# Kernel tuning notes

Measured on AMD Instinct MI355X. Metric: run time of the kernel, lower is better.

## Reference

```python
import jax, jax.numpy as jnp
import numpy as np

K = 5
PAD = 2  # same-size output: pad = dilation*(k-1)/2


def _patches(x, k, pad):
    # x: [B, C, H, W] -> [B, C, k, k, H', W'] (matches torch F.unfold + view layout)
    B, C, H, W = x.shape
    p = jax.lax.conv_general_dilated_patches(
        x, (k, k), (1, 1), [(pad, pad), (pad, pad)])
    return p.reshape(B, C, k, k, p.shape[-2], p.shape[-1])


def setup_inputs() -> dict:
    key = jax.random.key(0)
    k1, k2, k3, k4 = jax.random.split(key, 4)
    B, Cin, Cout, Cg, H, W = 4, 32, 32, 8, 128, 128
    x = jax.random.normal(k1, (B, Cin, H, W), jnp.float32)
    guide = jax.random.normal(k2, (B, Cg, H, W), jnp.float32)
    weight = jax.random.normal(k3, (Cout, Cin, K, K), jnp.float32) * 0.05
    bias = jax.random.normal(k4, (Cout,), jnp.float32) * 0.05
    return {"x": x, "guide": guide, "weight": weight, "bias": bias}


def reference(x, guide, weight, bias):
    k = weight.shape[-1]
    # --- packernel2d (gaussian, smooth_kernel_type='none', channel_wise=False) ---
    gp = _patches(guide, k, PAD)                      # [B, Cg, k, k, H, W]
    center = gp[:, :, k // 2, k // 2][:, :, None, None]  # self-tap feature
    d = gp - center
    kernel = jnp.exp(-0.5 * jnp.sum(d * d, axis=1, keepdims=True))  # [B,1,k,k,H,W]
    # --- pacconv2d native path ---
    cols = _patches(x, k, PAD)                        # [B, Cin, k, k, H, W]
    out = jnp.einsum('bjklmn,ojkl->bomn', cols * kernel, weight)
    return out + bias[None, :, None, None]
```

## Files before the change

kernel.cpp:

```cpp
#include <hip/hip_runtime.h>

#define Bn   4
#define CIN  32
#define COUT 32
#define CG   8
#define Hh   128
#define Ww   128
#define KK   5
#define HW   (Hh * Ww)

#define TW   64
#define TH   4
#define PRW  68
#define PRH  8
#define NSLOT (PRW * PRH)

typedef _Float16 h8  __attribute__((ext_vector_type(8)));
typedef _Float16 h2  __attribute__((ext_vector_type(2)));
typedef float    f4  __attribute__((ext_vector_type(4)));

#define XOFF  0
#define XJG   8704
#define WOFF  34816
#define KOFF  60416
#define SMEMB 73216

#define XT_OFF 0
#define WT_OFF 4194304
#define KW_OFF 4245504
#define WS_NEED 7522304

__global__ __launch_bounds__(512) void prep(
    const float* __restrict__ x, const float* __restrict__ guide,
    const float* __restrict__ w,
    _Float16* __restrict__ xt, _Float16* __restrict__ wt, _Float16* __restrict__ kw)
{
    const int bid = blockIdx.x;
    const int tid = threadIdx.x;

    if (bid < 512) {
        const int b = bid >> 7, m = bid & 127;
        const int n = tid & 127, jh = tid >> 7;
        const float* xp = x + ((size_t)(b * CIN + jh * 8)) * HW + m * Ww + n;
        h8 v;
#pragma unroll
        for (int e = 0; e < 8; ++e) v[e] = (_Float16)xp[(size_t)e * HW];
        ((h8*)xt)[((size_t)b * HW + m * Ww + n) * 4 + jh] = v;
    } else if (bid < 562) {
        const int idx = (bid - 512) * 512 + tid;
        const int ht = idx >> 9;
        const int half = ht / 25, t = ht - half * 25;
        const int rem = idx & 511;
        const int jg = rem >> 7, o = (rem >> 3) & 15, e = rem & 7;
        wt[idx] = (_Float16)w[(size_t)(half * 16 + o) * (CIN * KK * KK) + (jg * 8 + e) * (KK * KK) + t];
    } else {
        __shared__ __align__(16) _Float16 gl[NSLOT * 8];
        const int tb = bid - 562;
        const int tile = tb & 63, b = tb >> 6;
        const int tm = (tile >> 1) * TH, tn = (tile & 1) * TW;
        const float* gb = guide + (size_t)b * CG * HW;
#pragma unroll
        for (int it = 0; it < 2; ++it) {
            const int slot = it * 512 + tid;
            if (slot < NSLOT) {
                const int r = slot / PRW, c = slot - r * PRW;
                const int gm = tm + r - 2, gn = tn + c - 2;
                h8 v = {};
                if ((unsigned)gm < (unsigned)Hh && (unsigned)gn < (unsigned)Ww) {
#pragma unroll
                    for (int cg = 0; cg < 8; ++cg)
                        v[cg] = (_Float16)gb[(size_t)cg * HW + gm * Ww + gn];
                }
                *(h8*)(gl + slot * 8) = v;
            }
        }
        __syncthreads();
        const int px = tid & 255, th = tid >> 8;
        const int pr = px >> 6, pc = px & 63;
        const int pg = px >> 5, ps = (px >> 4) & 1, pi = px & 15;
        const h8 c8 = *(const h8*)(gl + ((pr + 2) * PRW + pc + 2) * 8);
        float cg[8];
#pragma unroll
        for (int i = 0; i < 8; ++i) cg[i] = (float)c8[i];
        _Float16* kout = kw + ((size_t)(b * 64 + tile) * 25) * 256;
        int t = 0;
#pragma unroll
        for (int k = 0; k < KK; ++k) {
#pragma unroll
            for (int l = 0; l < KK; ++l) {
                if ((t < 13) == (th == 0)) {
                    const h8 gv = *(const h8*)(gl + ((pr + k) * PRW + pc + l) * 8);
                    float ss = 0.f;
#pragma unroll
                    for (int i = 0; i < 8; ++i) {
                        const float d = (float)gv[i] - cg[i];
                        ss = fmaf(d, d, ss);
                    }
                    kout[t * 256 + (pg * 16 + pi) * 2 + ps] = (_Float16)__expf(-0.5f * ss);
                }
                ++t;
            }
        }
    }
}

__global__ __launch_bounds__(512, 4) void pac_mfma5(
    const _Float16* __restrict__ xt, const _Float16* __restrict__ wt,
    const _Float16* __restrict__ kw, const float* __restrict__ bias,
    float* __restrict__ out)
{
    __shared__ __align__(16) unsigned char smem[SMEMB];

    const int tid  = threadIdx.x;
    const int bx   = blockIdx.x;
    const int half = blockIdx.y;
    const int bz   = blockIdx.z;
    const int tm = (bx >> 1) * TH;
    const int tn = (bx & 1) * TW;

    const int pxbase = bz * HW;
#pragma unroll
    for (int it = 0; it < 5; ++it) {
        const int idx = it * 512 + tid;
        if (idx < 2176) {
            const int slot = idx >> 2, jg = idx & 3;
            const int r = slot / PRW;
            const int c = slot - r * PRW;
            const int gm = tm + r - 2, gn = tn + c - 2;
            h8 v = {};
            if ((unsigned)gm < (unsigned)Hh && (unsigned)gn < (unsigned)Ww)
                v = *(const h8*)(xt + ((size_t)(pxbase + gm * Ww + gn)) * 32 + jg * 8);
            *(h8*)(smem + XOFF + jg * XJG + slot * 16) = v;
        }
    }

    const h8* wth = (const h8*)(wt + half * 12800);
#pragma unroll
    for (int it = 0; it < 4; ++it) {
        const int idx = it * 512 + tid;
        if (idx < 1600)
            *(h8*)(smem + WOFF + idx * 16) = wth[idx];
    }

    const h8* ksrc = (const h8*)(kw + ((size_t)(bz * 64 + bx) * 25) * 256);
#pragma unroll
    for (int it = 0; it < 2; ++it) {
        const int idx = it * 512 + tid;
        if (idx < 800)
            *(h8*)(smem + KOFF + idx * 16) = ksrc[idx];
    }

    __syncthreads();

    const int lane = tid & 63;
    const int l15 = lane & 15, kg = lane >> 4;
    const int wv = tid >> 6;
    const int st0 = wv * 32, st1 = st0 + 16;
    const int r0 = wv >> 1;
    const int c00 = (wv & 1) * 32;

    f4 acc0 = {0.f, 0.f, 0.f, 0.f}, acc1 = {0.f, 0.f, 0.f, 0.f};
    const unsigned char* xg = smem + XOFF + kg * XJG;
    const int kbase = KOFF + (wv * 16 + l15) * 4;
    const float bv = bias[half * 16 + l15];

    int t = 0;
#pragma unroll
    for (int k = 0; k < KK; ++k) {
#pragma unroll
        for (int l = 0; l < KK; ++l) {
            const int abase = ((r0 + k) * PRW + c00 + l + l15) * 16;
            h8 A0 = *(const h8*)(xg + abase);
            h8 A1 = *(const h8*)(xg + abase + 256);
            h8 Bv = *(const h8*)(smem + WOFF + t * 1024 + kg * 256 + l15 * 16);
            h2 kk = *(const h2*)(smem + kbase + t * 512);

            h8 A0s = A0 * kk[0];
            h8 A1s = A1 * kk[1];

            acc0 = __builtin_amdgcn_mfma_f32_16x16x32_f16(A0s, Bv, acc0, 0, 0, 0);
            acc1 = __builtin_amdgcn_mfma_f32_16x16x32_f16(A1s, Bv, acc1, 0, 0, 0);
            ++t;
        }
    }

#pragma unroll
    for (int i = 0; i < 4; ++i) { acc0[i] += bv; acc1[i] += bv; }

    __syncthreads();
    float* outst = (float*)smem;
    *(f4*)(outst + l15 * 260 + st0 + kg * 4) = acc0;
    *(f4*)(outst + l15 * 260 + st1 + kg * 4) = acc1;
    __syncthreads();

    const int o = tid >> 5;
    const int p = (tid & 31) * 8;
    f4 v0 = *(const f4*)(outst + o * 260 + p);
    f4 v1 = *(const f4*)(outst + o * 260 + p + 4);
    const int mr = p >> 6, nc = p & 63;
    float* op = out + ((size_t)(bz * COUT + half * 16 + o)) * HW + (size_t)(tm + mr) * Ww + tn + nc;
    *(f4*)op = v0;
    *(f4*)(op + 4) = v1;
}

typedef _Float16 h4v __attribute__((ext_vector_type(4)));
__global__ __launch_bounds__(512, 4) void pac_mfma2(
    const float* __restrict__ x, const float* __restrict__ guide,
    const float* __restrict__ weight, const float* __restrict__ bias,
    float* __restrict__ out)
{
    __shared__ __align__(16) unsigned char smem[SMEMB];
    const int tid  = threadIdx.x;
    const int bx   = blockIdx.x;
    const int half = blockIdx.y;
    const int bz   = blockIdx.z;
    const int tm = (bx >> 1) * TH;
    const int tn = (bx & 1) * TW;

    const float* xb = x + (size_t)bz * CIN * HW;
#pragma unroll
    for (int it = 0; it < 34; ++it) {
        const int idx  = it * 512 + tid;
        const int j    = idx / NSLOT;
        const int slot = idx - j * NSLOT;
        const int r    = slot / PRW;
        const int c    = slot - r * PRW;
        const int gm = tm + r - 2, gn = tn + c - 2;
        float v = 0.f;
        if ((unsigned)gm < (unsigned)Hh && (unsigned)gn < (unsigned)Ww)
            v = xb[(size_t)j * HW + gm * Ww + gn];
        *(_Float16*)(smem + XOFF + (j >> 3) * XJG + slot * 16 + (j & 7) * 2) = (_Float16)v;
    }
#pragma unroll
    for (int it = 0; it < 25; ++it) {
        const int idx = it * 512 + tid;
        const int o = idx & 15;
        const int j = (idx >> 4) & 31;
        const int t = idx >> 9;
        const float v = weight[(size_t)(half * 16 + o) * (CIN * KK * KK) + j * (KK * KK) + t];
        *(_Float16*)(smem + WOFF + t * 1024 + (j >> 3) * 256 + o * 16 + (j & 7) * 2) = (_Float16)v;
    }
    {
        const int px = tid & 255, th = tid >> 8;
        const int pr = px >> 6, pc = px & 63;
        const int m = tm + pr, n = tn + pc;
        const float* gb = guide + ((size_t)bz * CG) * HW + m * Ww + n;
        float center[CG];
#pragma unroll
        for (int c = 0; c < CG; ++c) center[c] = gb[c * HW];
        int t = 0;
#pragma unroll
        for (int k = 0; k < KK; ++k) {
            const int dm = k - 2;
            const bool rowok = ((unsigned)(m + dm) < (unsigned)Hh);
#pragma unroll
            for (int l = 0; l < KK; ++l) {
                if ((t < 13) == (th == 0)) {
                    const int dn = l - 2;
                    const bool ok = rowok && ((unsigned)(n + dn) < (unsigned)Ww);
                    float ss = 0.f;
#pragma unroll
                    for (int c = 0; c < CG; ++c) {
                        float gv = ok ? gb[c * HW + dm * Ww + dn] : 0.f;
                        float d = gv - center[c];
                        ss = fmaf(d, d, ss);
                    }
                    *(_Float16*)(smem + KOFF + t * 512 + px * 2) = (_Float16)__expf(-0.5f * ss);
                }
                ++t;
            }
        }
    }
    __syncthreads();
    const int lane = tid & 63;
    const int l15 = lane & 15, kg = lane >> 4;
    const int wv = tid >> 6;
    const int st0 = wv * 32, st1 = st0 + 16;
    const int r0 = wv >> 1;
    const int c00 = (wv & 1) * 32;
    f4 acc0 = {0.f, 0.f, 0.f, 0.f}, acc1 = {0.f, 0.f, 0.f, 0.f};
    const unsigned char* xg = smem + XOFF + kg * XJG;
    const float bv = bias[half * 16 + l15];
    int t = 0;
#pragma unroll
    for (int k = 0; k < KK; ++k) {
#pragma unroll
        for (int l = 0; l < KK; ++l) {
            const int abase = ((r0 + k) * PRW + c00 + l + l15) * 16;
            h8 A0 = *(const h8*)(xg + abase);
            h8 A1 = *(const h8*)(xg + abase + 256);
            h8 Bv = *(const h8*)(smem + WOFF + t * 1024 + kg * 256 + l15 * 16);
            f4 p0 = __builtin_amdgcn_mfma_f32_16x16x32_f16(A0, Bv, (f4){0.f,0.f,0.f,0.f}, 0, 0, 0);
            f4 p1 = __builtin_amdgcn_mfma_f32_16x16x32_f16(A1, Bv, (f4){0.f,0.f,0.f,0.f}, 0, 0, 0);
            h4v k0 = *(const h4v*)(smem + KOFF + t * 512 + (st0 + kg * 4) * 2);
            h4v k1 = *(const h4v*)(smem + KOFF + t * 512 + (st1 + kg * 4) * 2);
#pragma unroll
            for (int i = 0; i < 4; ++i) {
                acc0[i] = fmaf((float)k0[i], p0[i], acc0[i]);
                acc1[i] = fmaf((float)k1[i], p1[i], acc1[i]);
            }
            ++t;
        }
    }
#pragma unroll
    for (int i = 0; i < 4; ++i) { acc0[i] += bv; acc1[i] += bv; }
    __syncthreads();
    float* outst = (float*)smem;
    *(f4*)(outst + l15 * 260 + st0 + kg * 4) = acc0;
    *(f4*)(outst + l15 * 260 + st1 + kg * 4) = acc1;
    __syncthreads();
    const int o = tid >> 5;
    const int p = (tid & 31) * 8;
    f4 v0 = *(const f4*)(outst + o * 260 + p);
    f4 v1 = *(const f4*)(outst + o * 260 + p + 4);
    const int mr = p >> 6, nc = p & 63;
    float* op = out + ((size_t)(bz * COUT + half * 16 + o)) * HW + (size_t)(tm + mr) * Ww + tn + nc;
    *(f4*)op = v0;
    *(f4*)(op + 4) = v1;
}

extern "C" void kernel_launch(void* const* d_in, const int* in_sizes, int n_in,
                              void* d_out, int out_size, void* d_ws, size_t ws_size,
                              hipStream_t stream) {
    const float* x      = (const float*)d_in[0];
    const float* guide  = (const float*)d_in[1];
    const float* weight = (const float*)d_in[2];
    const float* bias   = (const float*)d_in[3];
    float* out = (float*)d_out;

    if (ws_size >= (size_t)WS_NEED) {
        _Float16* xt = (_Float16*)((char*)d_ws + XT_OFF);
        _Float16* wt = (_Float16*)((char*)d_ws + WT_OFF);
        _Float16* kw = (_Float16*)((char*)d_ws + KW_OFF);
        prep<<<dim3(818), 512, 0, stream>>>(x, guide, weight, xt, wt, kw);
        pac_mfma5<<<dim3(64, 2, Bn), 512, 0, stream>>>(xt, wt, kw, bias, out);
    } else {
        pac_mfma2<<<dim3(64, 2, Bn), 512, 0, stream>>>(x, guide, weight, bias, out);
    }
}
```

Baseline: 23.64 us.

## Compute all output channels per block, second weight half in registers

The main MFMA kernel previously split the 32 output channels across two blocks, so each block reloaded and rescaled the same input patch tile and guidance kernel. Now one block computes all 32 output channels. The first half of the weights stays in shared memory and the second half is held in 25 register vectors per lane, which doubles MFMA work per loaded and scaled A fragment. The grid is halved and launch bounds drop to 2 blocks per CU. Register pressure rises sharply and occupancy and parallelism fall (256 blocks).

```diff
diff --git a/kernel.cpp b/kernel.cpp
--- a/kernel.cpp
+++ b/kernel.cpp
@@ -104,19 +104,27 @@
     }
 }
 
-__global__ __launch_bounds__(512, 4) void pac_mfma5(
+__global__ __launch_bounds__(512, 2) void pac_mfma6(
     const _Float16* __restrict__ xt, const _Float16* __restrict__ wt,
     const _Float16* __restrict__ kw, const float* __restrict__ bias,
     float* __restrict__ out)
 {
     __shared__ __align__(16) unsigned char smem[SMEMB];
 
-    const int tid  = threadIdx.x;
-    const int bx   = blockIdx.x;
-    const int half = blockIdx.y;
-    const int bz   = blockIdx.z;
+    const int tid = threadIdx.x;
+    const int bx  = blockIdx.x;
+    const int bz  = blockIdx.y;
     const int tm = (bx >> 1) * TH;
     const int tn = (bx & 1) * TW;
+
+    const int lane = tid & 63;
+    const int l15 = lane & 15, kg = lane >> 4;
+
+    const h8* wh1 = (const h8*)wt + 1600;
+    h8 B1r[25];
+#pragma unroll
+    for (int t = 0; t < 25; ++t)
+        B1r[t] = wh1[t * 64 + kg * 16 + l15];
 
     const int pxbase = bz * HW;
 #pragma unroll
@@ -134,7 +142,7 @@
         }
     }
 
-    const h8* wth = (const h8*)(wt + half * 12800);
+    const h8* wth = (const h8*)wt;
 #pragma unroll
     for (int it = 0; it < 4; ++it) {
         const int idx = it * 512 + tid;
@@ -152,17 +160,15 @@
 
     __syncthreads();
 
-    const int lane = tid & 63;
-    const int l15 = lane & 15, kg = lane >> 4;
     const int wv = tid >> 6;
     const int st0 = wv * 32, st1 = st0 + 16;
     const int r0 = wv >> 1;
     const int c00 = (wv & 1) * 32;
 
-    f4 acc0 = {0.f, 0.f, 0.f, 0.f}, acc1 = {0.f, 0.f, 0.f, 0.f};
+    f4 acc00 = {0.f,0.f,0.f,0.f}, acc01 = {0.f,0.f,0.f,0.f};
+    f4 acc10 = {0.f,0.f,0.f,0.f}, acc11 = {0.f,0.f,0.f,0.f};
     const unsigned char* xg = smem + XOFF + kg * XJG;
     const int kbase = KOFF + (wv * 16 + l15) * 4;
-    const float bv = bias[half * 16 + l15];
 
     int t = 0;
 #pragma unroll
@@ -172,35 +178,43 @@
             const int abase = ((r0 + k) * PRW + c00 + l + l15) * 16;
             h8 A0 = *(const h8*)(xg + abase);
             h8 A1 = *(const h8*)(xg + abase + 256);
-            h8 Bv = *(const h8*)(smem + WOFF + t * 1024 + kg * 256 + l15 * 16);
+            h8 B0 = *(const h8*)(smem + WOFF + t * 1024 + kg * 256 + l15 * 16);
             h2 kk = *(const h2*)(smem + kbase + t * 512);
 
             h8 A0s = A0 * kk[0];
             h8 A1s = A1 * kk[1];
 
-            acc0 = __builtin_amdgcn_mfma_f32_16x16x32_f16(A0s, Bv, acc0, 0, 0, 0);
-            acc1 = __builtin_amdgcn_mfma_f32_16x16x32_f16(A1s, Bv, acc1, 0, 0, 0);
+            acc00 = __builtin_amdgcn_mfma_f32_16x16x32_f16(A0s, B0,      acc00, 0, 0, 0);
+            acc01 = __builtin_amdgcn_mfma_f32_16x16x32_f16(A0s, B1r[t],  acc01, 0, 0, 0);
+            acc10 = __builtin_amdgcn_mfma_f32_16x16x32_f16(A1s, B0,      acc10, 0, 0, 0);
+            acc11 = __builtin_amdgcn_mfma_f32_16x16x32_f16(A1s, B1r[t],  acc11, 0, 0, 0);
             ++t;
         }
     }
 
-#pragma unroll
-    for (int i = 0; i < 4; ++i) { acc0[i] += bv; acc1[i] += bv; }
+    const float bv0 = bias[l15], bv1 = bias[16 + l15];
+#pragma unroll
+    for (int i = 0; i < 4; ++i) {
+        acc00[i] += bv0; acc10[i] += bv0;
+        acc01[i] += bv1; acc11[i] += bv1;
+    }
 
     __syncthreads();
     float* outst = (float*)smem;
-    *(f4*)(outst + l15 * 260 + st0 + kg * 4) = acc0;
-    *(f4*)(outst + l15 * 260 + st1 + kg * 4) = acc1;
-    __syncthreads();
-
-    const int o = tid >> 5;
-    const int p = (tid & 31) * 8;
-    f4 v0 = *(const f4*)(outst + o * 260 + p);
-    f4 v1 = *(const f4*)(outst + o * 260 + p + 4);
-    const int mr = p >> 6, nc = p & 63;
-    float* op = out + ((size_t)(bz * COUT + half * 16 + o)) * HW + (size_t)(tm + mr) * Ww + tn + nc;
-    *(f4*)op = v0;
-    *(f4*)(op + 4) = v1;
+    *(f4*)(outst + l15 * 260 + st0 + kg * 4) = acc00;
+    *(f4*)(outst + l15 * 260 + st1 + kg * 4) = acc10;
+    *(f4*)(outst + (16 + l15) * 260 + st0 + kg * 4) = acc01;
+    *(f4*)(outst + (16 + l15) * 260 + st1 + kg * 4) = acc11;
+    __syncthreads();
+
+    const int o = tid >> 4;
+    const int i = tid & 15;
+    float* op = out + ((size_t)(bz * COUT + o)) * HW;
+#pragma unroll
+    for (int c = 0; c < 4; ++c) {
+        f4 v = *(const f4*)(outst + o * 260 + c * 64 + i * 4);
+        *(f4*)(op + (size_t)(tm + c) * Ww + tn + i * 4) = v;
+    }
 }
 
 typedef _Float16 h4v __attribute__((ext_vector_type(4)));
@@ -333,7 +347,7 @@
         _Float16* wt = (_Float16*)((char*)d_ws + WT_OFF);
         _Float16* kw = (_Float16*)((char*)d_ws + KW_OFF);
         prep<<<dim3(818), 512, 0, stream>>>(x, guide, weight, xt, wt, kw);
-        pac_mfma5<<<dim3(64, 2, Bn), 512, 0, stream>>>(xt, wt, kw, bias, out);
+        pac_mfma6<<<dim3(64, Bn), 512, 0, stream>>>(xt, wt, kw, bias, out);
     } else {
         pac_mfma2<<<dim3(64, 2, Bn), 512, 0, stream>>>(x, guide, weight, bias, out);
     }
```

After: 23.60 us. Within noise of the previous version (-0.2%).
